# Performance work log

Measured on AMD Instinct MI355X. Metric: run time of the kernel, lower is better.

## Reference

```python
import jax, jax.numpy as jnp
import numpy as np

EPS = 1e-12  # torch F.normalize eps


def setup_inputs() -> dict:
    key = jax.random.key(0)
    k1, k2, k3 = jax.random.split(key, 3)
    B, D, H, W, K = 64, 512, 32, 32, 64
    x = jax.random.normal(k1, (B, D, H, W), dtype=jnp.float32)
    w = jax.random.normal(k2, (K, D), dtype=jnp.float32) * 0.05  # 1x1 conv weight
    c = jax.random.normal(k3, (K, D), dtype=jnp.float32)          # cluster centers
    return {"x": x, "w": w, "c": c}


def reference(x, w, c):
    B, D, H, W = x.shape
    K = w.shape[0]
    N = H * W
    # 1x1 conv (no bias): (B,D,H,W) x (K,D) -> (B,K,H,W)
    features = jnp.einsum('bdhw,kd->bkhw', x, w)
    # NOTE: original applies softmax over dim=2 (the H axis only)
    a_bar = jax.nn.softmax(features, axis=2)
    xf = x.reshape(B, D, N)
    a = a_bar.reshape(B, K, N)
    # V[b,k,d] = sum_n a[b,k,n] * (x[b,d,n] - c[k,d])
    V = jnp.einsum('bkn,bdn->bkd', a, xf) - a.sum(axis=2)[:, :, None] * c[None]
    V = V.transpose(2, 1, 0)  # (D, K, B)
    # F.normalize(V, p=2, dim=1) applied twice (second is idempotent)
    norm = jnp.maximum(jnp.linalg.norm(V, axis=1, keepdims=True), EPS)
    y = V / norm
    norm2 = jnp.maximum(jnp.linalg.norm(y, axis=1, keepdims=True), EPS)
    return y / norm2
```

## Files before the change

kernel.cpp:

```cpp
#include <hip/hip_runtime.h>


typedef __attribute__((ext_vector_type(8))) short short8;
typedef __attribute__((ext_vector_type(8))) unsigned short u16x8;
typedef __attribute__((ext_vector_type(4))) float f32x4;
typedef unsigned short u16;
typedef unsigned int u32;

__device__ __forceinline__ u16 f2bf(float f) {
  union { float f; u32 u; } v; v.f = f;
  u32 u = v.u;
  return (u16)((u + 0x7fffu + ((u >> 16) & 1u)) >> 16);
}

__global__ __launch_bounds__(256, 2) void k1_conv_softmax(
    const float* __restrict__ x, const float* __restrict__ wgt,
    u16* __restrict__ a_ws)
{
  const int blk = blockIdx.x;
  const int b  = blk & 63;
  const int wb = blk >> 6;
  const int w0 = wb * 4;
  const int tid  = threadIdx.x;
  const int lane = tid & 63;
  const int wv   = tid >> 6;

  __shared__ __align__(16) char smem[64 * 132 * 4];
  u16  (*as)[40] = (u16 (*)[40])smem;
  u16  (*bs)[40] = (u16 (*)[40])(smem + 5120);
  float (*F)[132] = (float (*)[132])smem;

  f32x4 acc[4][2];
#pragma unroll
  for (int mt = 0; mt < 4; mt++)
#pragma unroll
    for (int nt = 0; nt < 2; nt++) acc[mt][nt] = (f32x4){0.f, 0.f, 0.f, 0.f};

  const float* xb = x + (size_t)b * 512 * 1024;
  const int jw0 = wv * 32;
  const int row = lane & 15;
  const int q   = lane >> 4;
  const int ka = tid >> 2, sega = tid & 3;
  const int hh = tid >> 4, ddp = tid & 15;

  for (int d0 = 0; d0 < 512; d0 += 32) {
    {
      const float* src = wgt + ka * 512 + d0 + sega * 8;
      f32x4 f0 = *(const f32x4*)src;
      f32x4 f1 = *(const f32x4*)(src + 4);
      u16x8 t;
#pragma unroll
      for (int i = 0; i < 4; i++) { t[i] = f2bf(f0[i]); t[4 + i] = f2bf(f1[i]); }
      *(u16x8*)&as[ka][sega * 8] = t;
    }
#pragma unroll
    for (int i = 0; i < 2; i++) {
      const int h = hh * 2 + i;
      const float* px = xb + (size_t)(d0 + 2 * ddp) * 1024 + h * 32 + w0;
      f32x4 g0 = *(const f32x4*)px;
      f32x4 g1 = *(const f32x4*)(px + 1024);
      const int cb = ddp >> 2;
      const int co = (ddp & 3) * 2;
#pragma unroll
      for (int wl = 0; wl < 4; wl++) {
        const int j = h * 4 + wl;
        u32 p = (u32)f2bf(g0[wl]) | ((u32)f2bf(g1[wl]) << 16);
        *(u32*)&bs[j][((cb ^ wl) * 8) + co] = p;
      }
    }
    __syncthreads();
    short8 af[4];
#pragma unroll
    for (int mt = 0; mt < 4; mt++) af[mt] = *(const short8*)&as[mt * 16 + row][q * 8];
#pragma unroll
    for (int nt = 0; nt < 2; nt++) {
      const int j = jw0 + nt * 16 + row;
      short8 bf = *(const short8*)&bs[j][(q ^ (j & 3)) * 8];
#pragma unroll
      for (int mt = 0; mt < 4; mt++)
        acc[mt][nt] = __builtin_amdgcn_mfma_f32_16x16x32_bf16(af[mt], bf, acc[mt][nt], 0, 0, 0);
    }
    __syncthreads();
  }

#pragma unroll
  for (int mt = 0; mt < 4; mt++)
#pragma unroll
    for (int nt = 0; nt < 2; nt++) {
      const int j = jw0 + nt * 16 + row;
#pragma unroll
      for (int r = 0; r < 4; r++)
        F[mt * 16 + q * 4 + r][j] = acc[mt][nt][r];
    }
  __syncthreads();

  {
    const int k = tid >> 2, wl = tid & 3;
    float m = -1e30f;
#pragma unroll
    for (int h = 0; h < 32; h++) m = fmaxf(m, F[k][h * 4 + wl]);
    float s = 0.f;
#pragma unroll
    for (int h = 0; h < 32; h++) {
      float e = __expf(F[k][h * 4 + wl] - m);
      F[k][h * 4 + wl] = e;
      s += e;
    }
    const float inv = 1.0f / s;
    u16* arow = a_ws + ((size_t)b * 64 + k) * 1024 + w0 + wl;
#pragma unroll
    for (int h = 0; h < 32; h++)
      arow[h * 32] = f2bf(F[k][h * 4 + wl] * inv);
  }
}

__global__ __launch_bounds__(256, 2) void k2_aggregate(
    const float* __restrict__ x, const u16* __restrict__ a_ws,
    const float* __restrict__ cc, float* __restrict__ yw)
{
  const int blk = blockIdx.x;
  const int b  = blk & 63;
  const int db = blk >> 6;
  const int d0 = db * 64;
  const int tid  = threadIdx.x;
  const int lane = tid & 63;
  const int wv   = tid >> 6;

  __shared__ __align__(16) char smem[64 * 68 * 4 + 4 * 64 * 4 + 64 * 4];
  u16  (*as)[40] = (u16 (*)[40])smem;
  u16  (*bs)[40] = (u16 (*)[40])(smem + 5120);
  float (*V)[68] = (float (*)[68])smem;
  float* ss = (float*)(smem + 64 * 68 * 4);
  float* rs = ss + 256;

  f32x4 acc[4];
#pragma unroll
  for (int mt = 0; mt < 4; mt++) acc[mt] = (f32x4){0.f, 0.f, 0.f, 0.f};

  const float* xb = x + (size_t)b * 512 * 1024;
  const u16*   ab = a_ws + (size_t)b * 64 * 1024;
  const int row = lane & 15, q = lane >> 4;
  const int kr = tid >> 2, seg = tid & 3;

  for (int n0 = 0; n0 < 1024; n0 += 32) {
    *(u16x8*)&as[kr][seg * 8] = *(const u16x8*)(ab + kr * 1024 + n0 + seg * 8);
    {
      const float* px = xb + (size_t)(d0 + kr) * 1024 + n0 + seg * 8;
      f32x4 g0 = *(const f32x4*)px;
      f32x4 g1 = *(const f32x4*)(px + 4);
      u16x8 t;
#pragma unroll
      for (int i = 0; i < 4; i++) { t[i] = f2bf(g0[i]); t[4 + i] = f2bf(g1[i]); }
      *(u16x8*)&bs[kr][seg * 8] = t;
    }
    __syncthreads();
    short8 bf = *(const short8*)&bs[wv * 16 + row][q * 8];
#pragma unroll
    for (int mt = 0; mt < 4; mt++) {
      short8 af = *(const short8*)&as[mt * 16 + row][q * 8];
      acc[mt] = __builtin_amdgcn_mfma_f32_16x16x32_bf16(af, bf, acc[mt], 0, 0, 0);
    }
    __syncthreads();
  }

  {
    const int dl = wv * 16 + row;
#pragma unroll
    for (int mt = 0; mt < 4; mt++)
#pragma unroll
      for (int r = 0; r < 4; r++) {
        const int k = mt * 16 + q * 4 + r;
        V[k][dl] = acc[mt][r] - 32.0f * cc[k * 512 + d0 + dl];
      }
  }
  __syncthreads();
  {
    const int dl = tid & 63, part = tid >> 6;
    float s = 0.f;
#pragma unroll
    for (int r = 0; r < 16; r++) { const float v = V[part * 16 + r][dl]; s += v * v; }
    ss[part * 64 + dl] = s;
  }
  __syncthreads();
  if (tid < 64) {
    const float t = ss[tid] + ss[64 + tid] + ss[128 + tid] + ss[192 + tid];
    rs[tid] = 1.0f / fmaxf(sqrtf(t), 1e-12f);
  }
  __syncthreads();
  {
    const int dl = tid & 63, kg = tid >> 6;
    const float r = rs[dl];
    float* dst = yw + (size_t)b * 32768 + d0 + dl;
#pragma unroll
    for (int i = 0; i < 16; i++) {
      const int k = kg * 16 + i;
      dst[(size_t)k * 512] = V[k][dl] * r;
    }
  }
}

__global__ __launch_bounds__(256) void k3_transpose(
    const float* __restrict__ yw, float* __restrict__ out)
{
  const int blk = blockIdx.x;
  const int k  = blk & 63;
  const int dt = blk >> 6;
  const int d0 = dt * 64;
  const int tid = threadIdx.x;
  __shared__ float T[64][68];
  {
    const int bl = tid >> 2, seg = tid & 3;
    const float* src = yw + (size_t)bl * 32768 + k * 512 + d0 + seg * 16;
#pragma unroll
    for (int i = 0; i < 4; i++) {
      f32x4 v = *(const f32x4*)(src + i * 4);
#pragma unroll
      for (int jj = 0; jj < 4; jj++) T[seg * 16 + i * 4 + jj][bl] = v[jj];
    }
  }
  __syncthreads();
  {
    const int dl = tid >> 2, bseg = tid & 3;
    float* dst = out + (size_t)(d0 + dl) * 4096 + k * 64 + bseg * 16;
    const float* srcT = &T[dl][bseg * 16];
#pragma unroll
    for (int i = 0; i < 4; i++)
      *(f32x4*)(dst + i * 4) = *(const f32x4*)(srcT + i * 4);
  }
}

extern "C" void kernel_launch(void* const* d_in, const int* in_sizes, int n_in,
                              void* d_out, int out_size, void* d_ws, size_t ws_size,
                              hipStream_t stream) {
  const float* x = (const float*)d_in[0];
  const float* w = (const float*)d_in[1];
  const float* c = (const float*)d_in[2];
  float* out = (float*)d_out;
  u16*   a_ws = (u16*)d_ws;
  float* yw   = (float*)((char*)d_ws + (size_t)8 * 1024 * 1024);
  k1_conv_softmax<<<dim3(512), dim3(256), 0, stream>>>(x, w, a_ws);
  k2_aggregate<<<dim3(512), dim3(256), 0, stream>>>(x, a_ws, c, yw);
  k3_transpose<<<dim3(512), dim3(256), 0, stream>>>(yw, out);
}
```

Measured before the change: 241.7 us.

## Drop LDS staging in MFMA GEMMs, load fragments from global, split softmax kernel

Both GEMM kernels now load MFMA operand fragments straight from global memory into registers, with no shared-memory staging and no barriers. The conv kernel writes fp32 features to a workspace, and a separate softmax kernel does the H-axis softmax with wave shuffles. The aggregate kernel computes the per-d norm across k with xor shuffles instead of LDS reductions. This removes LDS traffic and syncs, but adds a fourth launch, a 16MB feature round-trip through memory, and strided scalar global loads of x in k1.

```diff
diff --git a/kernel.cpp b/kernel.cpp
--- a/kernel.cpp
+++ b/kernel.cpp
@@ -2,33 +2,34 @@
 
 
 typedef __attribute__((ext_vector_type(8))) short short8;
-typedef __attribute__((ext_vector_type(8))) unsigned short u16x8;
 typedef __attribute__((ext_vector_type(4))) float f32x4;
 typedef unsigned short u16;
 typedef unsigned int u32;
 
-__device__ __forceinline__ u16 f2bf(float f) {
-  union { float f; u32 u; } v; v.f = f;
-  u32 u = v.u;
-  return (u16)((u + 0x7fffu + ((u >> 16) & 1u)) >> 16);
-}
-
-__global__ __launch_bounds__(256, 2) void k1_conv_softmax(
+union S8u { u32 q[4]; short8 s; };
+
+__device__ __forceinline__ u32 pk2(float lo, float hi) {
+  union { float f; u32 u; } a, b; a.f = lo; b.f = hi;
+  u32 xl = (a.u + 0x7fffu + ((a.u >> 16) & 1u)) >> 16;
+  u32 xh = (b.u + 0x7fffu + ((b.u >> 16) & 1u)) & 0xffff0000u;
+  return xl | xh;
+}
+
+__device__ __forceinline__ u16 bf1(float f) {
+  union { float f; u32 u; } a; a.f = f;
+  return (u16)((a.u + 0x7fffu + ((a.u >> 16) & 1u)) >> 16);
+}
+
+__global__ __launch_bounds__(256, 2) void k1_features(
     const float* __restrict__ x, const float* __restrict__ wgt,
-    u16* __restrict__ a_ws)
+    float* __restrict__ feat)
 {
   const int blk = blockIdx.x;
-  const int b  = blk & 63;
-  const int wb = blk >> 6;
-  const int w0 = wb * 4;
-  const int tid  = threadIdx.x;
-  const int lane = tid & 63;
-  const int wv   = tid >> 6;
-
-  __shared__ __align__(16) char smem[64 * 132 * 4];
-  u16  (*as)[40] = (u16 (*)[40])smem;
-  u16  (*bs)[40] = (u16 (*)[40])(smem + 5120);
-  float (*F)[132] = (float (*)[132])smem;
+  const int b = blk & 63, ntile = blk >> 6;
+  const int tid = threadIdx.x, lane = tid & 63, wv = tid >> 6;
+  const int row = lane & 15, q = lane >> 4;
+  const int nb = ntile * 128 + wv * 32;
+  const float* xb = x + ((size_t)b << 19);
 
   f32x4 acc[4][2];
 #pragma unroll
@@ -36,174 +37,129 @@
 #pragma unroll
     for (int nt = 0; nt < 2; nt++) acc[mt][nt] = (f32x4){0.f, 0.f, 0.f, 0.f};
 
-  const float* xb = x + (size_t)b * 512 * 1024;
-  const int jw0 = wv * 32;
-  const int row = lane & 15;
-  const int q   = lane >> 4;
-  const int ka = tid >> 2, sega = tid & 3;
-  const int hh = tid >> 4, ddp = tid & 15;
-
+#pragma unroll 2
   for (int d0 = 0; d0 < 512; d0 += 32) {
+    short8 af[4];
+#pragma unroll
+    for (int mt = 0; mt < 4; mt++) {
+      const float* pw = wgt + (mt * 16 + row) * 512 + d0 + q * 8;
+      f32x4 w0 = *(const f32x4*)pw;
+      f32x4 w1 = *(const f32x4*)(pw + 4);
+      S8u t;
+      t.q[0] = pk2(w0[0], w0[1]); t.q[1] = pk2(w0[2], w0[3]);
+      t.q[2] = pk2(w1[0], w1[1]); t.q[3] = pk2(w1[2], w1[3]);
+      af[mt] = t.s;
+    }
+    short8 bf[2];
+#pragma unroll
+    for (int nt = 0; nt < 2; nt++) {
+      const float* px = xb + (size_t)(d0 + q * 8) * 1024 + nb + nt * 16 + row;
+      float v0 = px[0],    v1 = px[1024], v2 = px[2048], v3 = px[3072];
+      float v4 = px[4096], v5 = px[5120], v6 = px[6144], v7 = px[7168];
+      S8u t;
+      t.q[0] = pk2(v0, v1); t.q[1] = pk2(v2, v3);
+      t.q[2] = pk2(v4, v5); t.q[3] = pk2(v6, v7);
+      bf[nt] = t.s;
+    }
+#pragma unroll
+    for (int nt = 0; nt < 2; nt++)
+#pragma unroll
+      for (int mt = 0; mt < 4; mt++)
+        acc[mt][nt] = __builtin_amdgcn_mfma_f32_16x16x32_bf16(af[mt], bf[nt], acc[mt][nt], 0, 0, 0);
+  }
+  float* fb = feat + ((size_t)b << 16);
+#pragma unroll
+  for (int mt = 0; mt < 4; mt++)
+#pragma unroll
+    for (int nt = 0; nt < 2; nt++)
+#pragma unroll
+      for (int r = 0; r < 4; r++)
+        fb[(mt * 16 + q * 4 + r) * 1024 + nb + nt * 16 + row] = acc[mt][nt][r];
+}
+
+__global__ __launch_bounds__(256) void k1b_softmax(
+    const float* __restrict__ feat, u16* __restrict__ am)
+{
+  const int tid = threadIdx.x, lane = tid & 63, wv = tid >> 6;
+  const int rid = blockIdx.x * 4 + wv;
+  const float* f = feat + ((size_t)rid << 10);
+  u16* ar = am + ((size_t)rid << 10);
+  const int w = lane & 31, half = lane >> 5;
+  const int base = w + half * 512;
+  float v[16];
+  float m = -1e30f;
+#pragma unroll
+  for (int i = 0; i < 16; i++) { v[i] = f[base + i * 32]; m = fmaxf(m, v[i]); }
+  m = fmaxf(m, __shfl_xor(m, 32));
+  float s = 0.f;
+#pragma unroll
+  for (int i = 0; i < 16; i++) { v[i] = __expf(v[i] - m); s += v[i]; }
+  s += __shfl_xor(s, 32);
+  const float inv = 1.0f / s;
+#pragma unroll
+  for (int i = 0; i < 16; i++) ar[base + i * 32] = bf1(v[i] * inv);
+}
+
+__global__ __launch_bounds__(256, 2) void k2_aggregate(
+    const float* __restrict__ x, const u16* __restrict__ am,
+    const float* __restrict__ cc, float* __restrict__ yw)
+{
+  const int blk = blockIdx.x;
+  const int b = blk & 63, dt = blk >> 6;
+  const int tid = threadIdx.x, lane = tid & 63, wv = tid >> 6;
+  const int row = lane & 15, q = lane >> 4;
+  const int drow = dt * 64 + wv * 16 + row;
+  const float* xb = x + ((size_t)b << 19);
+  const u16* ab = am + ((size_t)b << 16);
+
+  f32x4 acc[4];
+#pragma unroll
+  for (int mt = 0; mt < 4; mt++) acc[mt] = (f32x4){0.f, 0.f, 0.f, 0.f};
+
+#pragma unroll 2
+  for (int n0 = 0; n0 < 1024; n0 += 32) {
+    short8 bfr;
     {
-      const float* src = wgt + ka * 512 + d0 + sega * 8;
-      f32x4 f0 = *(const f32x4*)src;
-      f32x4 f1 = *(const f32x4*)(src + 4);
-      u16x8 t;
-#pragma unroll
-      for (int i = 0; i < 4; i++) { t[i] = f2bf(f0[i]); t[4 + i] = f2bf(f1[i]); }
-      *(u16x8*)&as[ka][sega * 8] = t;
-    }
-#pragma unroll
-    for (int i = 0; i < 2; i++) {
-      const int h = hh * 2 + i;
-      const float* px = xb + (size_t)(d0 + 2 * ddp) * 1024 + h * 32 + w0;
-      f32x4 g0 = *(const f32x4*)px;
-      f32x4 g1 = *(const f32x4*)(px + 1024);
-      const int cb = ddp >> 2;
-      const int co = (ddp & 3) * 2;
-#pragma unroll
-      for (int wl = 0; wl < 4; wl++) {
-        const int j = h * 4 + wl;
-        u32 p = (u32)f2bf(g0[wl]) | ((u32)f2bf(g1[wl]) << 16);
-        *(u32*)&bs[j][((cb ^ wl) * 8) + co] = p;
-      }
-    }
-    __syncthreads();
-    short8 af[4];
-#pragma unroll
-    for (int mt = 0; mt < 4; mt++) af[mt] = *(const short8*)&as[mt * 16 + row][q * 8];
-#pragma unroll
-    for (int nt = 0; nt < 2; nt++) {
-      const int j = jw0 + nt * 16 + row;
-      short8 bf = *(const short8*)&bs[j][(q ^ (j & 3)) * 8];
-#pragma unroll
-      for (int mt = 0; mt < 4; mt++)
-        acc[mt][nt] = __builtin_amdgcn_mfma_f32_16x16x32_bf16(af[mt], bf, acc[mt][nt], 0, 0, 0);
-    }
-    __syncthreads();
-  }
-
-#pragma unroll
-  for (int mt = 0; mt < 4; mt++)
-#pragma unroll
-    for (int nt = 0; nt < 2; nt++) {
-      const int j = jw0 + nt * 16 + row;
-#pragma unroll
-      for (int r = 0; r < 4; r++)
-        F[mt * 16 + q * 4 + r][j] = acc[mt][nt][r];
-    }
-  __syncthreads();
-
-  {
-    const int k = tid >> 2, wl = tid & 3;
-    float m = -1e30f;
-#pragma unroll
-    for (int h = 0; h < 32; h++) m = fmaxf(m, F[k][h * 4 + wl]);
-    float s = 0.f;
-#pragma unroll
-    for (int h = 0; h < 32; h++) {
-      float e = __expf(F[k][h * 4 + wl] - m);
-      F[k][h * 4 + wl] = e;
-      s += e;
-    }
-    const float inv = 1.0f / s;
-    u16* arow = a_ws + ((size_t)b * 64 + k) * 1024 + w0 + wl;
-#pragma unroll
-    for (int h = 0; h < 32; h++)
-      arow[h * 32] = f2bf(F[k][h * 4 + wl] * inv);
-  }
-}
-
-__global__ __launch_bounds__(256, 2) void k2_aggregate(
-    const float* __restrict__ x, const u16* __restrict__ a_ws,
-    const float* __restrict__ cc, float* __restrict__ yw)
-{
-  const int blk = blockIdx.x;
-  const int b  = blk & 63;
-  const int db = blk >> 6;
-  const int d0 = db * 64;
-  const int tid  = threadIdx.x;
-  const int lane = tid & 63;
-  const int wv   = tid >> 6;
-
-  __shared__ __align__(16) char smem[64 * 68 * 4 + 4 * 64 * 4 + 64 * 4];
-  u16  (*as)[40] = (u16 (*)[40])smem;
-  u16  (*bs)[40] = (u16 (*)[40])(smem + 5120);
-  float (*V)[68] = (float (*)[68])smem;
-  float* ss = (float*)(smem + 64 * 68 * 4);
-  float* rs = ss + 256;
-
-  f32x4 acc[4];
-#pragma unroll
-  for (int mt = 0; mt < 4; mt++) acc[mt] = (f32x4){0.f, 0.f, 0.f, 0.f};
-
-  const float* xb = x + (size_t)b * 512 * 1024;
-  const u16*   ab = a_ws + (size_t)b * 64 * 1024;
-  const int row = lane & 15, q = lane >> 4;
-  const int kr = tid >> 2, seg = tid & 3;
-
-  for (int n0 = 0; n0 < 1024; n0 += 32) {
-    *(u16x8*)&as[kr][seg * 8] = *(const u16x8*)(ab + kr * 1024 + n0 + seg * 8);
-    {
-      const float* px = xb + (size_t)(d0 + kr) * 1024 + n0 + seg * 8;
+      const float* px = xb + (size_t)drow * 1024 + n0 + q * 8;
       f32x4 g0 = *(const f32x4*)px;
       f32x4 g1 = *(const f32x4*)(px + 4);
-      u16x8 t;
-#pragma unroll
-      for (int i = 0; i < 4; i++) { t[i] = f2bf(g0[i]); t[4 + i] = f2bf(g1[i]); }
-      *(u16x8*)&bs[kr][seg * 8] = t;
-    }
-    __syncthreads();
-    short8 bf = *(const short8*)&bs[wv * 16 + row][q * 8];
+      S8u t;
+      t.q[0] = pk2(g0[0], g0[1]); t.q[1] = pk2(g0[2], g0[3]);
+      t.q[2] = pk2(g1[0], g1[1]); t.q[3] = pk2(g1[2], g1[3]);
+      bfr = t.s;
+    }
 #pragma unroll
     for (int mt = 0; mt < 4; mt++) {
-      short8 af = *(const short8*)&as[mt * 16 + row][q * 8];
-      acc[mt] = __builtin_amdgcn_mfma_f32_16x16x32_bf16(af, bf, acc[mt], 0, 0, 0);
-    }
-    __syncthreads();
-  }
-
-  {
-    const int dl = wv * 16 + row;
-#pragma unroll
-    for (int mt = 0; mt < 4; mt++)
-#pragma unroll
-      for (int r = 0; r < 4; r++) {
-        const int k = mt * 16 + q * 4 + r;
-        V[k][dl] = acc[mt][r] - 32.0f * cc[k * 512 + d0 + dl];
-      }
-  }
-  __syncthreads();
-  {
-    const int dl = tid & 63, part = tid >> 6;
-    float s = 0.f;
-#pragma unroll
-    for (int r = 0; r < 16; r++) { const float v = V[part * 16 + r][dl]; s += v * v; }
-    ss[part * 64 + dl] = s;
-  }
-  __syncthreads();
-  if (tid < 64) {
-    const float t = ss[tid] + ss[64 + tid] + ss[128 + tid] + ss[192 + tid];
-    rs[tid] = 1.0f / fmaxf(sqrtf(t), 1e-12f);
-  }
-  __syncthreads();
-  {
-    const int dl = tid & 63, kg = tid >> 6;
-    const float r = rs[dl];
-    float* dst = yw + (size_t)b * 32768 + d0 + dl;
-#pragma unroll
-    for (int i = 0; i < 16; i++) {
-      const int k = kg * 16 + i;
-      dst[(size_t)k * 512] = V[k][dl] * r;
-    }
-  }
+      short8 af = *(const short8*)(ab + (mt * 16 + row) * 1024 + n0 + q * 8);
+      acc[mt] = __builtin_amdgcn_mfma_f32_16x16x32_bf16(af, bfr, acc[mt], 0, 0, 0);
+    }
+  }
+  const int dcol = dt * 64 + wv * 16 + row;
+  float v[16]; float ss = 0.f;
+#pragma unroll
+  for (int mt = 0; mt < 4; mt++)
+#pragma unroll
+    for (int r = 0; r < 4; r++) {
+      const int k = mt * 16 + q * 4 + r;
+      const float t = acc[mt][r] - 32.0f * cc[k * 512 + dcol];
+      v[mt * 4 + r] = t; ss += t * t;
+    }
+  ss += __shfl_xor(ss, 16);
+  ss += __shfl_xor(ss, 32);
+  const float rn = 1.0f / fmaxf(sqrtf(ss), 1e-12f);
+  float* yb = yw + ((size_t)b << 15) + dcol;
+#pragma unroll
+  for (int mt = 0; mt < 4; mt++)
+#pragma unroll
+    for (int r = 0; r < 4; r++)
+      yb[(size_t)(mt * 16 + q * 4 + r) << 9] = v[mt * 4 + r] * rn;
 }
 
 __global__ __launch_bounds__(256) void k3_transpose(
     const float* __restrict__ yw, float* __restrict__ out)
 {
   const int blk = blockIdx.x;
-  const int k  = blk & 63;
+  const int k = blk & 63;
   const int dt = blk >> 6;
   const int d0 = dt * 64;
   const int tid = threadIdx.x;
@@ -236,9 +192,11 @@
   const float* w = (const float*)d_in[1];
   const float* c = (const float*)d_in[2];
   float* out = (float*)d_out;
-  u16*   a_ws = (u16*)d_ws;
-  float* yw   = (float*)((char*)d_ws + (size_t)8 * 1024 * 1024);
-  k1_conv_softmax<<<dim3(512), dim3(256), 0, stream>>>(x, w, a_ws);
-  k2_aggregate<<<dim3(512), dim3(256), 0, stream>>>(x, a_ws, c, yw);
-  k3_transpose<<<dim3(512), dim3(256), 0, stream>>>(yw, out);
-}
+  float* feat = (float*)d_ws;
+  u16*   a_ws = (u16*)((char*)d_ws + (size_t)16 * 1024 * 1024);
+  float* yw   = (float*)((char*)d_ws + (size_t)24 * 1024 * 1024);
+  k1_features <<<dim3(512),  dim3(256), 0, stream>>>(x, w, feat);
+  k1b_softmax <<<dim3(1024), dim3(256), 0, stream>>>(feat, a_ws);
+  k2_aggregate<<<dim3(512),  dim3(256), 0, stream>>>(x, a_ws, c, yw);
+  k3_transpose<<<dim3(512),  dim3(256), 0, stream>>>(yw, out);
+}
```

Result: slower. 274.4 us (+13.5%).
